# Optimization experiments

Hardware: AMD Instinct MI355X
Metric: run time of the kernel (lower is better)

The kernel has to match this reference:

```python
import jax, jax.numpy as jnp
import numpy as np

EPS = 1e-13

def setup_inputs() -> dict:
    key = jax.random.key(0)
    k1, k2, k3 = jax.random.split(key, 3)
    B, L, H = 64, 512, 1024
    sentence = jax.random.normal(k1, (B, L, H), dtype=jnp.float32)
    mask = jax.random.uniform(k2, (B, L), dtype=jnp.float32)
    attention_matrix = jax.random.normal(k3, (B, L, L), dtype=jnp.float32)
    return {"sentence": sentence, "mask": mask, "attention_matrix": attention_matrix}

def reference(sentence, mask, attention_matrix):
    # stable softmax over last dim of [B, L, L]
    attention_weights = jax.nn.softmax(attention_matrix, axis=-1)
    # mask rows: mask is [B, L] -> [B, L, 1]
    attention_weights = attention_weights * mask[:, :, None]
    # renormalize over last dim
    attention_weights = attention_weights / (attention_weights.sum(-1, keepdims=True) + EPS)
    # weighted sum: [B, L, L] @ [B, L, H] -> [B, L, H]
    return jnp.einsum('bij,bjh->bih', attention_weights, sentence)
```

## Files before the change

kernel.cpp:

```cpp
#include <hip/hip_runtime.h>
#include <hip/hip_bf16.h>

#define B_ 64
#define L_ 512
#define H_ 1024
#define EPS_ 1e-13f

typedef unsigned short u16;
typedef __attribute__((ext_vector_type(8))) short s16x8;
typedef __attribute__((ext_vector_type(4))) float f32x4;

__device__ __forceinline__ u16 f2bf(float f) {
  __hip_bfloat16 h = __float2bfloat16(f);
  union { __hip_bfloat16 h; u16 u; } c; c.h = h; return c.u;
}

__global__ __launch_bounds__(256) void softmax_rows(const float* __restrict__ att,
                                                    const float* __restrict__ mask,
                                                    u16* __restrict__ Wout) {
  const int w = threadIdx.x >> 6, lane = threadIdx.x & 63;
  const int row0 = blockIdx.x * 16 + w * 4;

  float a[4][8];
#pragma unroll
  for (int r = 0; r < 4; ++r) {
    const float* p = att + (size_t)(row0 + r) * L_ + lane * 8;
    float4 v0 = *(const float4*)p;
    float4 v1 = *(const float4*)(p + 4);
    a[r][0] = v0.x; a[r][1] = v0.y; a[r][2] = v0.z; a[r][3] = v0.w;
    a[r][4] = v1.x; a[r][5] = v1.y; a[r][6] = v1.z; a[r][7] = v1.w;
  }

  float m[4];
#pragma unroll
  for (int r = 0; r < 4; ++r) {
    m[r] = a[r][0];
#pragma unroll
    for (int j = 1; j < 8; ++j) m[r] = fmaxf(m[r], a[r][j]);
  }
#pragma unroll
  for (int off = 32; off > 0; off >>= 1)
#pragma unroll
    for (int r = 0; r < 4; ++r) m[r] = fmaxf(m[r], __shfl_xor(m[r], off));

  float z[4] = {0.f, 0.f, 0.f, 0.f};
#pragma unroll
  for (int r = 0; r < 4; ++r)
#pragma unroll
    for (int j = 0; j < 8; ++j) { a[r][j] = __expf(a[r][j] - m[r]); z[r] += a[r][j]; }
#pragma unroll
  for (int off = 32; off > 0; off >>= 1)
#pragma unroll
    for (int r = 0; r < 4; ++r) z[r] += __shfl_xor(z[r], off);

#pragma unroll
  for (int r = 0; r < 4; ++r) {
    const float mk = mask[row0 + r];
    const float c = (1.0f / z[r]) * (mk / (mk + EPS_));
    union { u16 u[8]; uint4 v; } wv;
#pragma unroll
    for (int j = 0; j < 8; ++j) wv.u[j] = f2bf(a[r][j] * c);
    *(uint4*)(Wout + (size_t)(row0 + r) * L_ + lane * 8) = wv.v;
  }
}

#define GLOAD(gp, lp)                                                              \
  __builtin_amdgcn_global_load_lds((const __attribute__((address_space(1))) unsigned*)(gp), \
                                   (__attribute__((address_space(3))) unsigned*)(void*)(lp), 16, 0, 0)

__global__ __launch_bounds__(512, 2) void gemm_xd(const u16* __restrict__ Wm,
                                                  const float* __restrict__ X,
                                                  float* __restrict__ out) {
  const int NT = 16;
  const int swz = (blockIdx.x & 7) * 64 + (blockIdx.x >> 3);
  const int b  = swz >> 3;
  const int mt = (swz >> 2) & 1;
  const int nt = swz & 3;

  __shared__ __align__(16) char lds[81920];

  const int t = threadIdx.x;
  const int lane = t & 63;
  const int w = t >> 6;
  const int wm = w >> 2, wn = w & 3;

  const u16* gW = Wm + ((size_t)b * L_ + mt * 256) * L_;
  const float* gX = X + (size_t)b * L_ * H_ + nt * 256;

  const int r0 = t >> 2;
  const int xsw = (r0 & 3) ^ ((r0 >> 2) & 3);
  const int scol = ((t & 3) ^ xsw) * 8;
  const u16* pA0 = gW + (size_t)r0 * L_ + scol;
  char* dA = lds + w * 1024;

  const int bn = t & 255;
  const int kg0 = (t >> 8) * 2;
  const float* pX0 = gX + bn;

  int offA[8], offB[4];
#pragma unroll
  for (int mf = 0; mf < 8; ++mf) {
    int r = wm * 128 + mf * 16 + (lane & 15);
    offA[mf] = r * 64 + ((((lane >> 4) ^ (r & 3) ^ ((r >> 2) & 3))) << 4);
  }
#pragma unroll
  for (int nf = 0; nf < 4; ++nf) {
    int r = wn * 64 + nf * 16 + (lane & 15);
    offB[nf] = 49152 + r * 64 + ((((lane >> 4) ^ ((r >> 2) & 3))) << 4);
  }

  f32x4 acc[8][4] = {};
  float bx[2][2][8];

#define A_ISSUE(tt)                                                       \
  do {                                                                    \
    GLOAD(pA0 + (tt) * 32, dA + ((tt) % 3) * 16384);                      \
    GLOAD(pA0 + (tt) * 32 + 128 * (size_t)L_, dA + ((tt) % 3) * 16384 + 8192); \
  } while (0)

#define B_ISSUE(tt)                                                       \
  do {                                                                    \
    _Pragma("unroll")                                                     \
    for (int g = 0; g < 2; ++g)                                           \
      _Pragma("unroll")                                                   \
      for (int j = 0; j < 8; ++j)                                         \
        bx[(tt) & 1][g][j] = pX0[(size_t)((tt) * 32 + (kg0 + g) * 8 + j) * H_]; \
  } while (0)

#define B_CVT_WRITE(tt)                                                   \
  do {                                                                    \
    _Pragma("unroll")                                                     \
    for (int g = 0; g < 2; ++g) {                                         \
      union { u16 u[8]; uint4 v; } pk;                                    \
      _Pragma("unroll")                                                   \
      for (int j = 0; j < 8; ++j) pk.u[j] = f2bf(bx[(tt) & 1][g][j]);     \
      int kg = kg0 + g;                                                   \
      *(uint4*)(lds + 49152 + ((tt) & 1) * 16384 + bn * 64 +              \
                ((kg ^ ((bn >> 2) & 3)) << 4)) = pk.v;                    \
    }                                                                     \
  } while (0)

  A_ISSUE(0); B_ISSUE(0); A_ISSUE(1); B_ISSUE(1);
  asm volatile("s_waitcnt vmcnt(18)" ::: "memory");
  B_CVT_WRITE(0);
  asm volatile("s_waitcnt lgkmcnt(0)" ::: "memory");
  __builtin_amdgcn_s_barrier();

#pragma unroll
  for (int k = 0; k < NT; ++k) {
    if (k + 2 < NT) { A_ISSUE(k + 2); B_ISSUE(k + 2); }

    const char* baseA = lds + (k % 3) * 16384;
    const char* baseB = lds + (k & 1) * 16384;
    s16x8 af[8], bf4[4];
#pragma unroll
    for (int mf = 0; mf < 8; ++mf) af[mf] = *(const s16x8*)(baseA + offA[mf]);
#pragma unroll
    for (int nf = 0; nf < 4; ++nf) bf4[nf] = *(const s16x8*)(baseB + offB[nf]);
    asm volatile("s_waitcnt lgkmcnt(0)" ::: "memory");

    __builtin_amdgcn_s_setprio(1);
#pragma unroll
    for (int mf = 0; mf < 8; ++mf)
#pragma unroll
      for (int nf = 0; nf < 4; ++nf)
        acc[mf][nf] = __builtin_amdgcn_mfma_f32_16x16x32_bf16(af[mf], bf4[nf], acc[mf][nf], 0, 0, 0);
    __builtin_amdgcn_s_setprio(0);

    if (k + 1 < NT) {
      if (k + 2 < NT) asm volatile("s_waitcnt vmcnt(18)" ::: "memory");
      else            asm volatile("s_waitcnt vmcnt(0)" ::: "memory");
      B_CVT_WRITE(k + 1);
      asm volatile("s_waitcnt lgkmcnt(0)" ::: "memory");
      __builtin_amdgcn_s_barrier();
    }
  }
#undef A_ISSUE
#undef B_ISSUE
#undef B_CVT_WRITE

  const int orow0 = mt * 256 + wm * 128 + ((lane >> 4) << 2);
  const int ocol0 = nt * 256 + wn * 64 + (lane & 15);
#pragma unroll
  for (int mf = 0; mf < 8; ++mf)
#pragma unroll
    for (int nf = 0; nf < 4; ++nf)
#pragma unroll
      for (int j = 0; j < 4; ++j) {
        int row = orow0 + mf * 16 + j;
        int col = ocol0 + nf * 16;
        out[((size_t)b * L_ + row) * H_ + col] = acc[mf][nf][j];
      }
}

extern "C" void kernel_launch(void* const* d_in, const int* in_sizes, int n_in,
                              void* d_out, int out_size, void* d_ws, size_t ws_size,
                              hipStream_t stream) {
  (void)in_sizes; (void)n_in; (void)out_size; (void)ws_size;
  const float* sent = (const float*)d_in[0];
  const float* mask = (const float*)d_in[1];
  const float* att  = (const float*)d_in[2];
  u16* Wm = (u16*)d_ws;
  float* outp = (float*)d_out;

  softmax_rows<<<2048, 256, 0, stream>>>(att, mask, Wm);
  gemm_xd<<<B_ * 2 * 4, 512, 0, stream>>>(Wm, sent, outp);
}
```

Before: 96.13 us.

## Deepen X prefetch, vectorize fp32 loads to float2, split A fragment loads

Each thread now loads two adjacent fp32 columns of X with float2 loads instead of scalar loads, and X prefetch is raised to three stages (register ring of 3) so global loads are issued one extra K-tile ahead. The A fragment LDS reads are split into two halves of four, each followed by its 16 MFMAs, which cuts register pressure and lets LDS reads overlap compute. The vmcnt wait counts are retuned for the new issue pattern. The risk is higher register use from the extra bx stage, and wrong vmcnt values could cause a race or a stall.

```diff
diff --git a/kernel.cpp b/kernel.cpp
--- a/kernel.cpp
+++ b/kernel.cpp
@@ -93,9 +93,11 @@
   const u16* pA0 = gW + (size_t)r0 * L_ + scol;
   char* dA = lds + w * 1024;
 
-  const int bn = t & 255;
-  const int kg0 = (t >> 8) * 2;
-  const float* pX0 = gX + bn;
+  const int n0 = (t & 127) * 2;
+  const int oq = t >> 7;
+  const float* pX0 = gX + n0;
+  const int wadr0 = 49152 + n0 * 64 + ((oq ^ ((n0 >> 2) & 3)) << 4);
+  const int wadr1 = 49152 + (n0 + 1) * 64 + ((oq ^ (((n0 + 1) >> 2) & 3)) << 4);
 
   int offA[8], offB[4];
 #pragma unroll
@@ -110,7 +112,7 @@
   }
 
   f32x4 acc[8][4] = {};
-  float bx[2][2][8];
+  float2 bx[3][8];
 
 #define A_ISSUE(tt)                                                       \
   do {                                                                    \
@@ -121,26 +123,23 @@
 #define B_ISSUE(tt)                                                       \
   do {                                                                    \
     _Pragma("unroll")                                                     \
-    for (int g = 0; g < 2; ++g)                                           \
-      _Pragma("unroll")                                                   \
-      for (int j = 0; j < 8; ++j)                                         \
-        bx[(tt) & 1][g][j] = pX0[(size_t)((tt) * 32 + (kg0 + g) * 8 + j) * H_]; \
+    for (int j = 0; j < 8; ++j)                                           \
+      bx[(tt) % 3][j] = *(const float2*)(pX0 + (size_t)((tt) * 32 + oq * 8 + j) * H_); \
   } while (0)
 
 #define B_CVT_WRITE(tt)                                                   \
   do {                                                                    \
+    union { u16 u[8]; uint4 v; } p0, p1;                                  \
     _Pragma("unroll")                                                     \
-    for (int g = 0; g < 2; ++g) {                                         \
-      union { u16 u[8]; uint4 v; } pk;                                    \
-      _Pragma("unroll")                                                   \
-      for (int j = 0; j < 8; ++j) pk.u[j] = f2bf(bx[(tt) & 1][g][j]);     \
-      int kg = kg0 + g;                                                   \
-      *(uint4*)(lds + 49152 + ((tt) & 1) * 16384 + bn * 64 +              \
-                ((kg ^ ((bn >> 2) & 3)) << 4)) = pk.v;                    \
+    for (int j = 0; j < 8; ++j) {                                         \
+      p0.u[j] = f2bf(bx[(tt) % 3][j].x);                                  \
+      p1.u[j] = f2bf(bx[(tt) % 3][j].y);                                  \
     }                                                                     \
+    *(uint4*)(lds + ((tt) & 1) * 16384 + wadr0) = p0.v;                   \
+    *(uint4*)(lds + ((tt) & 1) * 16384 + wadr1) = p1.v;                   \
   } while (0)
 
-  A_ISSUE(0); B_ISSUE(0); A_ISSUE(1); B_ISSUE(1);
+  A_ISSUE(0); B_ISSUE(0); A_ISSUE(1); B_ISSUE(1); B_ISSUE(2);
   asm volatile("s_waitcnt vmcnt(18)" ::: "memory");
   B_CVT_WRITE(0);
   asm volatile("s_waitcnt lgkmcnt(0)" ::: "memory");
@@ -148,28 +147,42 @@
 
 #pragma unroll
   for (int k = 0; k < NT; ++k) {
-    if (k + 2 < NT) { A_ISSUE(k + 2); B_ISSUE(k + 2); }
+    if (k + 2 < NT) A_ISSUE(k + 2);
+    if (k + 3 < NT) B_ISSUE(k + 3);
 
     const char* baseA = lds + (k % 3) * 16384;
     const char* baseB = lds + (k & 1) * 16384;
-    s16x8 af[8], bf4[4];
-#pragma unroll
-    for (int mf = 0; mf < 8; ++mf) af[mf] = *(const s16x8*)(baseA + offA[mf]);
+    s16x8 af[4], bf4[4];
 #pragma unroll
     for (int nf = 0; nf < 4; ++nf) bf4[nf] = *(const s16x8*)(baseB + offB[nf]);
+#pragma unroll
+    for (int mf = 0; mf < 4; ++mf) af[mf] = *(const s16x8*)(baseA + offA[mf]);
     asm volatile("s_waitcnt lgkmcnt(0)" ::: "memory");
 
     __builtin_amdgcn_s_setprio(1);
 #pragma unroll
-    for (int mf = 0; mf < 8; ++mf)
+    for (int mf = 0; mf < 4; ++mf)
 #pragma unroll
       for (int nf = 0; nf < 4; ++nf)
         acc[mf][nf] = __builtin_amdgcn_mfma_f32_16x16x32_bf16(af[mf], bf4[nf], acc[mf][nf], 0, 0, 0);
     __builtin_amdgcn_s_setprio(0);
 
+#pragma unroll
+    for (int mf = 0; mf < 4; ++mf) af[mf] = *(const s16x8*)(baseA + offA[mf + 4]);
+    asm volatile("s_waitcnt lgkmcnt(0)" ::: "memory");
+
+    __builtin_amdgcn_s_setprio(1);
+#pragma unroll
+    for (int mf = 0; mf < 4; ++mf)
+#pragma unroll
+      for (int nf = 0; nf < 4; ++nf)
+        acc[mf + 4][nf] = __builtin_amdgcn_mfma_f32_16x16x32_bf16(af[mf], bf4[nf], acc[mf + 4][nf], 0, 0, 0);
+    __builtin_amdgcn_s_setprio(0);
+
     if (k + 1 < NT) {
-      if (k + 2 < NT) asm volatile("s_waitcnt vmcnt(18)" ::: "memory");
-      else            asm volatile("s_waitcnt vmcnt(0)" ::: "memory");
+      if (k <= 12)      asm volatile("s_waitcnt vmcnt(18)" ::: "memory");
+      else if (k == 13) asm volatile("s_waitcnt vmcnt(10)" ::: "memory");
+      else              asm volatile("s_waitcnt vmcnt(0)" ::: "memory");
       B_CVT_WRITE(k + 1);
       asm volatile("s_waitcnt lgkmcnt(0)" ::: "memory");
       __builtin_amdgcn_s_barrier();
```

Measured after the change: 101.7 us. +5.8%, slower.

## Load fp32 sentence tiles directly to LDS and convert to bf16 on read

Applied to the files above, without the earlier changes.

The B operand (sentence) is now moved by async global_load_lds DMA into a triple-buffered fp32 LDS region instead of register loads followed by bf16 conversion and LDS writes. Conversion to bf16 happens when fragments are read from LDS, using scalar 4-byte reads with an XOR swizzle. This removes register staging and the extra write/wait step, but raises LDS use to 144KB, which drops occupancy to one block per CU. It also replaces each vector fragment read with eight scalar LDS reads plus conversions, executed redundantly by every wave.

```diff
diff --git a/kernel.cpp b/kernel.cpp
--- a/kernel.cpp
+++ b/kernel.cpp
@@ -77,7 +77,7 @@
   const int mt = (swz >> 2) & 1;
   const int nt = swz & 3;
 
-  __shared__ __align__(16) char lds[81920];
+  __shared__ __align__(16) char lds[147456];
 
   const int t = threadIdx.x;
   const int lane = t & 63;
@@ -93,57 +93,43 @@
   const u16* pA0 = gW + (size_t)r0 * L_ + scol;
   char* dA = lds + w * 1024;
 
-  const int bn = t & 255;
-  const int kg0 = (t >> 8) * 2;
-  const float* pX0 = gX + bn;
-
-  int offA[8], offB[4];
+  const float* pXw = gX + (size_t)w * H_;
+  const int l4  = lane * 4;
+  const int lx4 = (lane ^ 4) * 4;
+  char* dBw = lds + 49152 + w * 1024;
+
+  int offA[8];
 #pragma unroll
   for (int mf = 0; mf < 8; ++mf) {
     int r = wm * 128 + mf * 16 + (lane & 15);
     offA[mf] = r * 64 + ((((lane >> 4) ^ (r & 3) ^ ((r >> 2) & 3))) << 4);
   }
+  int offBc[4];
 #pragma unroll
   for (int nf = 0; nf < 4; ++nf) {
-    int r = wn * 64 + nf * 16 + (lane & 15);
-    offB[nf] = 49152 + r * 64 + ((((lane >> 4) ^ ((r >> 2) & 3))) << 4);
+    int n = wn * 64 + nf * 16 + (lane & 15);
+    int oct = lane >> 4;
+    offBc[nf] = oct * 8192 + ((n ^ ((oct & 1) << 4)) << 2);
   }
 
   f32x4 acc[8][4] = {};
-  float bx[2][2][8];
-
-#define A_ISSUE(tt)                                                       \
-  do {                                                                    \
-    GLOAD(pA0 + (tt) * 32, dA + ((tt) % 3) * 16384);                      \
+
+#define A_ISSUE(tt)                                                        \
+  do {                                                                     \
+    GLOAD(pA0 + (tt) * 32, dA + ((tt) % 3) * 16384);                       \
     GLOAD(pA0 + (tt) * 32 + 128 * (size_t)L_, dA + ((tt) % 3) * 16384 + 8192); \
   } while (0)
 
-#define B_ISSUE(tt)                                                       \
-  do {                                                                    \
-    _Pragma("unroll")                                                     \
-    for (int g = 0; g < 2; ++g)                                           \
-      _Pragma("unroll")                                                   \
-      for (int j = 0; j < 8; ++j)                                         \
-        bx[(tt) & 1][g][j] = pX0[(size_t)((tt) * 32 + (kg0 + g) * 8 + j) * H_]; \
+#define B_ISSUE(tt)                                                        \
+  do {                                                                     \
+    GLOAD(pXw + (size_t)((tt) * 32 + 0)  * H_ + l4,  dBw + ((tt) % 3) * 32768);         \
+    GLOAD(pXw + (size_t)((tt) * 32 + 8)  * H_ + lx4, dBw + ((tt) % 3) * 32768 + 8192);  \
+    GLOAD(pXw + (size_t)((tt) * 32 + 16) * H_ + l4,  dBw + ((tt) % 3) * 32768 + 16384); \
+    GLOAD(pXw + (size_t)((tt) * 32 + 24) * H_ + lx4, dBw + ((tt) % 3) * 32768 + 24576); \
   } while (0)
 
-#define B_CVT_WRITE(tt)                                                   \
-  do {                                                                    \
-    _Pragma("unroll")                                                     \
-    for (int g = 0; g < 2; ++g) {                                         \
-      union { u16 u[8]; uint4 v; } pk;                                    \
-      _Pragma("unroll")                                                   \
-      for (int j = 0; j < 8; ++j) pk.u[j] = f2bf(bx[(tt) & 1][g][j]);     \
-      int kg = kg0 + g;                                                   \
-      *(uint4*)(lds + 49152 + ((tt) & 1) * 16384 + bn * 64 +              \
-                ((kg ^ ((bn >> 2) & 3)) << 4)) = pk.v;                    \
-    }                                                                     \
-  } while (0)
-
   A_ISSUE(0); B_ISSUE(0); A_ISSUE(1); B_ISSUE(1);
-  asm volatile("s_waitcnt vmcnt(18)" ::: "memory");
-  B_CVT_WRITE(0);
-  asm volatile("s_waitcnt lgkmcnt(0)" ::: "memory");
+  asm volatile("s_waitcnt vmcnt(6)" ::: "memory");
   __builtin_amdgcn_s_barrier();
 
 #pragma unroll
@@ -151,12 +137,21 @@
     if (k + 2 < NT) { A_ISSUE(k + 2); B_ISSUE(k + 2); }
 
     const char* baseA = lds + (k % 3) * 16384;
-    const char* baseB = lds + (k & 1) * 16384;
-    s16x8 af[8], bf4[4];
+    const char* baseB = lds + 49152 + (k % 3) * 32768;
+
+    s16x8 af[8];
 #pragma unroll
     for (int mf = 0; mf < 8; ++mf) af[mf] = *(const s16x8*)(baseA + offA[mf]);
-#pragma unroll
-    for (int nf = 0; nf < 4; ++nf) bf4[nf] = *(const s16x8*)(baseB + offB[nf]);
+
+    s16x8 bf4[4];
+#pragma unroll
+    for (int nf = 0; nf < 4; ++nf) {
+      union { u16 u[8]; s16x8 v; } pk;
+#pragma unroll
+      for (int j = 0; j < 8; ++j)
+        pk.u[j] = f2bf(*(const float*)(baseB + offBc[nf] + j * 1024));
+      bf4[nf] = pk.v;
+    }
     asm volatile("s_waitcnt lgkmcnt(0)" ::: "memory");
 
     __builtin_amdgcn_s_setprio(1);
@@ -168,16 +163,13 @@
     __builtin_amdgcn_s_setprio(0);
 
     if (k + 1 < NT) {
-      if (k + 2 < NT) asm volatile("s_waitcnt vmcnt(18)" ::: "memory");
+      if (k + 2 < NT) asm volatile("s_waitcnt vmcnt(6)" ::: "memory");
       else            asm volatile("s_waitcnt vmcnt(0)" ::: "memory");
-      B_CVT_WRITE(k + 1);
-      asm volatile("s_waitcnt lgkmcnt(0)" ::: "memory");
       __builtin_amdgcn_s_barrier();
     }
   }
 #undef A_ISSUE
 #undef B_ISSUE
-#undef B_CVT_WRITE
 
   const int orow0 = mt * 256 + wm * 128 + ((lane >> 4) << 2);
   const int ocol0 = nt * 256 + wn * 64 + (lane & 15);
```

Result: faster. 93.75 us, median of 2 (-2.5%).
